# Performance work log

Hardware: AMD Instinct MI355X
Metric: run time of the kernel (lower is better)

## Reference

```python
import jax, jax.numpy as jnp
import numpy as np


def setup_inputs() -> dict:
    key = jax.random.key(0)
    k1, k2, k3 = jax.random.split(key, 3)
    B, T, E = 4, 2048, 1024
    x = jax.random.normal(k1, (B, T, E), dtype=jnp.float32)
    # torch nn.Linear weight layout: [out_features, in_features]
    w_qkv = jax.random.normal(k2, (3 * E, E), dtype=jnp.float32) * (E ** -0.5)
    w_out = jax.random.normal(k3, (E, E), dtype=jnp.float32) * (E ** -0.5)
    return {"x": x, "w_qkv": w_qkv, "w_out": w_out}


def reference(x, w_qkv, w_out):
    B, T, E = x.shape
    H = 16
    D = E // H  # head_dim
    # QKV projection (Linear, bias=False): x @ W.T -> [B,T,3E]
    qkv = jnp.einsum('bte,fe->btf', x, w_qkv)
    qkv = qkv.reshape(B, T, 3, H, D).transpose(2, 0, 3, 1, 4)  # [3,B,H,T,D]
    q, k, v = qkv[0], qkv[1], qkv[2]
    scale = 1.0 / jnp.sqrt(jnp.asarray(D, dtype=x.dtype))
    att = jnp.einsum('bhqd,bhkd->bhqk', q, k) * scale  # [B,H,T,T]
    causal = jnp.tril(jnp.ones((T, T), dtype=bool))
    att = jnp.where(causal[None, None], att, jnp.asarray(-jnp.inf, dtype=att.dtype))
    att = jax.nn.softmax(att, axis=-1)
    # dropout = 0.0 (eval-mode): identity
    y = jnp.einsum('bhqk,bhkd->bhqd', att, v)  # [B,H,T,D]
    y = y.transpose(0, 2, 1, 3).reshape(B, T, E)
    return jnp.einsum('bte,fe->btf', y, w_out)
```

## Files before the change

### kernel.cpp

```cpp
#include <hip/hip_runtime.h>

typedef __bf16 bf16x8 __attribute__((ext_vector_type(8)));
typedef __bf16 bf16x4 __attribute__((ext_vector_type(4)));
typedef __bf16 bf16x2 __attribute__((ext_vector_type(2)));
typedef float f32x4 __attribute__((ext_vector_type(4)));
typedef float f32x16 __attribute__((ext_vector_type(16)));
typedef unsigned short ushortx8 __attribute__((ext_vector_type(8)));
typedef unsigned short ushortx4 __attribute__((ext_vector_type(4)));
typedef unsigned int uint32x4v __attribute__((ext_vector_type(4)));

#define DEVI static __device__ __forceinline__

DEVI unsigned short f2bf(float f) {
  unsigned int u = __builtin_bit_cast(unsigned int, f);
  u += 0x7FFFu + ((u >> 16) & 1u);
  return (unsigned short)(u >> 16);
}

DEVI bf16x8 ld8(const unsigned short* p) {
  return __builtin_bit_cast(bf16x8, *(const ushortx8*)p);
}

DEVI void gll16(const unsigned short* g, unsigned short* l) {
  __builtin_amdgcn_global_load_lds((const __attribute__((address_space(1))) void*)g,
                                   (__attribute__((address_space(3))) void*)l, 16, 0, 0);
}

#define MFMA16(a, b, c) __builtin_amdgcn_mfma_f32_16x16x32_bf16(a, b, c, 0, 0, 0)
#define MFMA32(a, b, c) __builtin_amdgcn_mfma_f32_32x32x16_bf16(a, b, c, 0, 0, 0)

DEVI unsigned pkbf(float lo, float hi) {
  bf16x2 v;
  v[0] = (__bf16)lo;
  v[1] = (__bf16)hi;
  return __builtin_bit_cast(unsigned, v);
}

DEVI float swaphalf_max(float x) {
  unsigned xu = __builtin_bit_cast(unsigned, x);
  auto pr = __builtin_amdgcn_permlane32_swap(xu, xu, false, false);
  return fmaxf(__builtin_bit_cast(float, (unsigned)pr[0]),
               __builtin_bit_cast(float, (unsigned)pr[1]));
}

DEVI float swaphalf_add(float x) {
  unsigned xu = __builtin_bit_cast(unsigned, x);
  auto pr = __builtin_amdgcn_permlane32_swap(xu, xu, false, false);
  return __builtin_bit_cast(float, (unsigned)pr[0]) +
         __builtin_bit_cast(float, (unsigned)pr[1]);
}

DEVI bf16x8 ldswz(const unsigned short* L, int row, int colsh) {
  return ld8(L + row * 64 + ((((colsh * 2) ^ ((row & 7) << 4))) >> 1));
}

#define SB 4
#define ST 2048
#define SE 1024
#define SH 16
#define SD 64
#define QSCALE 0.18033688011112042f
#define DMTHR 11.541560327111708f

#define NXq4   2097152
#define NQKVq4  786432
#define NWOq4   262144

__global__ void cvt_all(const float* __restrict__ x, const float* __restrict__ wq,
                        const float* __restrict__ wo,
                        unsigned short* __restrict__ xb, unsigned short* __restrict__ wqb,
                        unsigned short* __restrict__ wob) {
  int i = blockIdx.x * blockDim.x + threadIdx.x;
  const float* src;
  unsigned short* dst;
  int j;
  if (i < NXq4) { src = x; dst = xb; j = i; }
  else if (i < NXq4 + NQKVq4) { src = wq; dst = wqb; j = i - NXq4; }
  else { src = wo; dst = wob; j = i - NXq4 - NQKVq4; }
  float4 v = ((const float4*)src)[j];
  ushortx4 o;
  o.x = f2bf(v.x); o.y = f2bf(v.y); o.z = f2bf(v.z); o.w = f2bf(v.w);
  ((ushortx4*)dst)[j] = o;
}

template<int EPI>
__global__ __launch_bounds__(512, 2) void gemm_big(
    const unsigned short* __restrict__ A, const unsigned short* __restrict__ Bw,
    float* __restrict__ Cf,
    unsigned short* __restrict__ Qo, unsigned short* __restrict__ Ko,
    unsigned short* __restrict__ VTo,
    int M, int N, int K) {
  __shared__ unsigned short As[2][256 * 64];
  __shared__ unsigned short Bs[2][256 * 64];
  const int tid = threadIdx.x;
  const int lane = tid & 63;
  const int w = tid >> 6;
  const int wr = w >> 2, wc = w & 3;
  const int r16 = lane & 15, g = lane >> 4;

  const int nwg = gridDim.x * gridDim.y;
  const int lin = blockIdx.x + blockIdx.y * gridDim.x;
  const int wg = (lin & 7) * (nwg >> 3) + (lin >> 3);
  const int bx = wg % gridDim.x, by = wg / gridDim.x;
  const int m0 = by * 256, n0 = bx * 256;

  f32x4 acc[8][4] = {};

  auto stage = [&](int kt, int buf) {
    const int k0 = kt << 6;
#pragma unroll
    for (int it = 0; it < 4; ++it) {
      int c = it * 512 + tid;
      int row = c >> 3, j = c & 7;
      int src = ((j * 16) ^ ((row & 7) << 4)) >> 1;
      gll16(A + (size_t)(m0 + row) * K + k0 + src, As[buf] + c * 8);
    }
#pragma unroll
    for (int it = 0; it < 4; ++it) {
      int c = it * 512 + tid;
      int row = c >> 3, j = c & 7;
      int src = ((j * 16) ^ ((row & 7) << 4)) >> 1;
      gll16(Bw + (size_t)(n0 + row) * K + k0 + src, Bs[buf] + c * 8);
    }
  };

  const int ntk = K >> 6;
  stage(0, 0);
  stage(1, 1);
  asm volatile("s_waitcnt vmcnt(8)" ::: "memory");
  __builtin_amdgcn_s_barrier();
  __builtin_amdgcn_sched_barrier(0);

  int cur = 0;
  for (int t = 0; t < ntk; ++t) {
    const unsigned short* Ab = As[cur];
    const unsigned short* Bb = Bs[cur];

    bf16x8 af[8][2], bfr[4][2];
#pragma unroll
    for (int m = 0; m < 8; ++m)
#pragma unroll
      for (int ks = 0; ks < 2; ++ks)
        af[m][ks] = ldswz(Ab, wr * 128 + m * 16 + r16, ks * 32 + g * 8);
#pragma unroll
    for (int n = 0; n < 4; ++n)
#pragma unroll
      for (int ks = 0; ks < 2; ++ks)
        bfr[n][ks] = ldswz(Bb, wc * 64 + n * 16 + r16, ks * 32 + g * 8);

    __builtin_amdgcn_s_setprio(1);
#pragma unroll
    for (int m = 0; m < 8; ++m)
#pragma unroll
      for (int n = 0; n < 4; ++n)
        acc[m][n] = MFMA16(af[m][0], bfr[n][0], acc[m][n]);
    __builtin_amdgcn_s_setprio(0);

    asm volatile("s_waitcnt lgkmcnt(0)" ::: "memory");
    __builtin_amdgcn_s_barrier();
    __builtin_amdgcn_sched_barrier(0);

    if (t + 2 < ntk) stage(t + 2, cur);
    __builtin_amdgcn_sched_barrier(0);

    __builtin_amdgcn_s_setprio(1);
#pragma unroll
    for (int m = 0; m < 8; ++m)
#pragma unroll
      for (int n = 0; n < 4; ++n)
        acc[m][n] = MFMA16(af[m][1], bfr[n][1], acc[m][n]);
    __builtin_amdgcn_s_setprio(0);

    if (t + 1 < ntk) {
      if (t + 2 < ntk) asm volatile("s_waitcnt vmcnt(8)" ::: "memory");
      else             asm volatile("s_waitcnt vmcnt(0)" ::: "memory");
      __builtin_amdgcn_s_barrier();
      __builtin_amdgcn_sched_barrier(0);
    }
    cur ^= 1;
  }

  if (EPI == 0) {
#pragma unroll
    for (int mt = 0; mt < 8; ++mt)
#pragma unroll
      for (int nt2 = 0; nt2 < 4; ++nt2)
#pragma unroll
        for (int r = 0; r < 4; ++r) {
          int m = m0 + wr * 128 + mt * 16 + g * 4 + r;
          int n = n0 + wc * 64 + nt2 * 16 + r16;
          Cf[(size_t)m * N + n] = acc[mt][nt2][r];
        }
  } else {
    const int which = (n0 + wc * 64) >> 10;
#pragma unroll
    for (int mt = 0; mt < 8; ++mt) {
      const int tb = m0 + wr * 128 + mt * 16 + g * 4;
      const int b = tb >> 11, t = tb & (ST - 1);
#pragma unroll
      for (int nt2 = 0; nt2 < 4; ++nt2) {
        int n = n0 + wc * 64 + nt2 * 16 + r16;
        int h = (n >> 6) & (SH - 1), d = n & (SD - 1);
        int bh = b * SH + h;
        if (which == 2) {
          ushortx4 o;
#pragma unroll
          for (int r = 0; r < 4; ++r) o[r] = f2bf(acc[mt][nt2][r]);
          *(ushortx4*)&VTo[((size_t)bh * SD + d) * ST + t] = o;
        } else if (which == 0) {
#pragma unroll
          for (int r = 0; r < 4; ++r)
            Qo[((size_t)bh * ST + t + r) * SD + d] = f2bf(acc[mt][nt2][r] * QSCALE);
        } else {
#pragma unroll
          for (int r = 0; r < 4; ++r)
            Ko[((size_t)bh * ST + t + r) * SD + d] = f2bf(acc[mt][nt2][r]);
        }
      }
    }
  }
}

__global__ __launch_bounds__(256, 2) void gemm_sm(
    const unsigned short* __restrict__ A, const unsigned short* __restrict__ Bw,
    float* __restrict__ Cf, int M, int N, int K) {
  __shared__ unsigned short As[128 * 64];
  __shared__ unsigned short Bs[128 * 64];
  const int tid = threadIdx.x;
  const int lane = tid & 63;
  const int w = tid >> 6;
  const int wr = w >> 1, wc = w & 1;
  const int r16 = lane & 15, g = lane >> 4;

  const int nwg = gridDim.x * gridDim.y;
  const int lin = blockIdx.x + blockIdx.y * gridDim.x;
  const int wg = (lin & 7) * (nwg >> 3) + (lin >> 3);
  const int bx = wg % gridDim.x, by = wg / gridDim.x;
  const int m0 = by * 128, n0 = bx * 128;

  f32x4 acc[4][4] = {};

  for (int k0 = 0; k0 < K; k0 += 64) {
    __syncthreads();
#pragma unroll
    for (int it = 0; it < 4; ++it) {
      int c = it * 256 + tid;
      int row = c >> 3, j = c & 7;
      int src = ((j * 16) ^ ((row & 7) << 4)) >> 1;
      gll16(A + (size_t)(m0 + row) * K + k0 + src, As + c * 8);
    }
#pragma unroll
    for (int it = 0; it < 4; ++it) {
      int c = it * 256 + tid;
      int row = c >> 3, j = c & 7;
      int src = ((j * 16) ^ ((row & 7) << 4)) >> 1;
      gll16(Bw + (size_t)(n0 + row) * K + k0 + src, Bs + c * 8);
    }
    __syncthreads();
#pragma unroll
    for (int ks = 0; ks < 2; ++ks) {
      bf16x8 af[4], bfr[4];
#pragma unroll
      for (int mt = 0; mt < 4; ++mt)
        af[mt] = ldswz(As, wr * 64 + mt * 16 + r16, ks * 32 + g * 8);
#pragma unroll
      for (int nt2 = 0; nt2 < 4; ++nt2)
        bfr[nt2] = ldswz(Bs, wc * 64 + nt2 * 16 + r16, ks * 32 + g * 8);
#pragma unroll
      for (int mt = 0; mt < 4; ++mt)
#pragma unroll
        for (int nt2 = 0; nt2 < 4; ++nt2)
          acc[mt][nt2] = MFMA16(af[mt], bfr[nt2], acc[mt][nt2]);
    }
  }

#pragma unroll
  for (int mt = 0; mt < 4; ++mt)
#pragma unroll
    for (int nt2 = 0; nt2 < 4; ++nt2)
#pragma unroll
      for (int r = 0; r < 4; ++r) {
        int m = m0 + wr * 64 + mt * 16 + g * 4 + r;
        int n = n0 + wc * 64 + nt2 * 16 + r16;
        Cf[(size_t)m * N + n] = acc[mt][nt2][r];
      }
}


DEVI void stage_tile(const unsigned short* gbase, size_t rowstride,
                     unsigned short* lds, int tid) {
#pragma unroll
  for (int it = 0; it < 2; ++it) {
    int c = it * 256 + tid;
    int row = c >> 3, j = c & 7;
    int src = ((j * 16) ^ ((row & 7) << 4)) >> 1;
    gll16(gbase + (size_t)row * rowstride + src, lds + c * 8);
  }
}

__global__ __launch_bounds__(256, 4) void attn_causal(
    const unsigned short* __restrict__ Q, const unsigned short* __restrict__ Kv,
    const unsigned short* __restrict__ VT, unsigned short* __restrict__ Y) {
  __shared__ unsigned short Ks[2][64 * 64];
  __shared__ unsigned short Vs[2][64 * 64];

  const int tid = threadIdx.x;
  const int lane = tid & 63;
  const int w = tid >> 6;
  const int l5 = lane & 31, h = lane >> 5;

  const int lin = blockIdx.x + blockIdx.y * gridDim.x;
  const int xcd = lin & 7;
  const int idx = lin >> 3;
  const int qt = (ST / 128 - 1) - (idx >> 3);
  const int bh = xcd + 8 * (idx & 7);
  const size_t base = (size_t)bh * ST * SD;

  const int q_glob = qt * 128 + w * 32 + l5;
  const int qwmin = qt * 128 + w * 32;

  bf16x8 qf[4];
#pragma unroll
  for (int kk = 0; kk < 4; ++kk)
    qf[kk] = ld8(Q + base + (size_t)q_glob * SD + kk * 16 + h * 8);

  float mrow = -__builtin_inff();
  float lrow = 0.f;
  f32x16 acc[2] = {};

  const int nkv = 2 * qt + 2;
  stage_tile(Kv + base, SD, Ks[0], tid);
  stage_tile(VT + base, ST, Vs[0], tid);
  __syncthreads();

  for (int kvt = 0; kvt < nkv; ++kvt) {
    const int cur = kvt & 1;
    if (kvt + 1 < nkv) {
      stage_tile(Kv + base + (size_t)(kvt + 1) * 64 * SD, SD, Ks[cur ^ 1], tid);
      stage_tile(VT + base + (kvt + 1) * 64, ST, Vs[cur ^ 1], tid);
    }

    const bool active = (kvt * 64) <= (qwmin + 31);
    if (active) {
      f32x16 s0 = {}, s1 = {};
      __builtin_amdgcn_s_setprio(1);
#pragma unroll
      for (int kk = 0; kk < 4; ++kk) {
        bf16x8 k0 = ldswz(Ks[cur], l5, kk * 16 + h * 8);
        s0 = MFMA32(k0, qf[kk], s0);
      }
#pragma unroll
      for (int kk = 0; kk < 4; ++kk) {
        bf16x8 k1 = ldswz(Ks[cur], 32 + l5, kk * 16 + h * 8);
        s1 = MFMA32(k1, qf[kk], s1);
      }
      __builtin_amdgcn_s_setprio(0);

      if (kvt * 64 + 63 > qwmin) {
        const int t0 = kvt * 64 + 4 * h;
#pragma unroll
        for (int reg = 0; reg < 16; ++reg) {
          int t = t0 + (reg & 3) + 8 * (reg >> 2);
          if (t > q_glob) s0[reg] = -__builtin_inff();
          if (t + 32 > q_glob) s1[reg] = -__builtin_inff();
        }
      }

      f32x16 mx;
#pragma unroll
      for (int i = 0; i < 16; ++i) mx[i] = fmaxf(s0[i], s1[i]);
#pragma unroll
      for (int i = 0; i < 8; ++i) mx[i] = fmaxf(mx[i], mx[i + 8]);
#pragma unroll
      for (int i = 0; i < 4; ++i) mx[i] = fmaxf(mx[i], mx[i + 4]);
      float bm = fmaxf(fmaxf(mx[0], mx[1]), fmaxf(mx[2], mx[3]));
      bm = swaphalf_max(bm);

      if (__any(bm > mrow + DMTHR)) {
        float mn = fmaxf(mrow, bm);
        float corr = exp2f(mrow - mn);
        mrow = mn;
        lrow *= corr;
#pragma unroll
        for (int dblk = 0; dblk < 2; ++dblk)
#pragma unroll
          for (int i = 0; i < 16; ++i) acc[dblk][i] *= corr;
      }

#pragma unroll
      for (int i = 0; i < 16; ++i) {
        s0[i] = exp2f(s0[i] - mrow);
        s1[i] = exp2f(s1[i] - mrow);
      }
      f32x16 sm;
#pragma unroll
      for (int i = 0; i < 16; ++i) sm[i] = s0[i] + s1[i];
#pragma unroll
      for (int i = 0; i < 8; ++i) sm[i] += sm[i + 8];
#pragma unroll
      for (int i = 0; i < 4; ++i) sm[i] += sm[i + 4];
      float rs = (sm[0] + sm[1]) + (sm[2] + sm[3]);
      lrow += swaphalf_add(rs);

      bf16x8 pb[2][2];
      auto packblk = [&](const f32x16& S, bf16x8* out) {
        unsigned a = pkbf(S[0], S[1]), b2 = pkbf(S[2], S[3]);
        unsigned c = pkbf(S[4], S[5]), d2 = pkbf(S[6], S[7]);
        auto r0 = __builtin_amdgcn_permlane32_swap(a, c, false, false);
        auto r1 = __builtin_amdgcn_permlane32_swap(b2, d2, false, false);
        uint32x4v w0 = {(unsigned)r0[0], (unsigned)r1[0], (unsigned)r0[1], (unsigned)r1[1]};
        out[0] = __builtin_bit_cast(bf16x8, w0);
        unsigned e = pkbf(S[8], S[9]), f2 = pkbf(S[10], S[11]);
        unsigned g2 = pkbf(S[12], S[13]), h2 = pkbf(S[14], S[15]);
        auto r2 = __builtin_amdgcn_permlane32_swap(e, g2, false, false);
        auto r3 = __builtin_amdgcn_permlane32_swap(f2, h2, false, false);
        uint32x4v w1 = {(unsigned)r2[0], (unsigned)r3[0], (unsigned)r2[1], (unsigned)r3[1]};
        out[1] = __builtin_bit_cast(bf16x8, w1);
      };
      packblk(s0, pb[0]);
      packblk(s1, pb[1]);

      __builtin_amdgcn_s_setprio(1);
#pragma unroll
      for (int dblk = 0; dblk < 2; ++dblk)
#pragma unroll
        for (int tt = 0; tt < 2; ++tt)
#pragma unroll
          for (int sl = 0; sl < 2; ++sl) {
            bf16x8 va = ldswz(Vs[cur], dblk * 32 + l5, tt * 32 + sl * 16 + h * 8);
            acc[dblk] = MFMA32(va, pb[tt][sl], acc[dblk]);
          }
      __builtin_amdgcn_s_setprio(0);
    }

    __syncthreads();
  }

  const int b = bh >> 4, hd = bh & 15;
  const float inv = 1.f / lrow;
#pragma unroll
  for (int dblk = 0; dblk < 2; ++dblk)
#pragma unroll
    for (int rg = 0; rg < 4; ++rg) {
      bf16x4 o;
#pragma unroll
      for (int j = 0; j < 4; ++j) o[j] = (__bf16)(acc[dblk][rg * 4 + j] * inv);
      int d = dblk * 32 + rg * 8 + 4 * h;
      *(ushortx4*)&Y[((size_t)b * ST + q_glob) * SE + hd * SD + d] =
          __builtin_bit_cast(ushortx4, o);
    }
}

extern "C" void kernel_launch(void* const* d_in, const int* in_sizes, int n_in,
                              void* d_out, int out_size, void* d_ws, size_t ws_size,
                              hipStream_t stream) {
  const float* x = (const float*)d_in[0];
  const float* w_qkv = (const float*)d_in[1];
  const float* w_out = (const float*)d_in[2];
  float* out = (float*)d_out;

  const size_t NX = (size_t)SB * ST * SE;
  const size_t NQKV = (size_t)3 * SE * SE;
  const size_t NWO = (size_t)SE * SE;
  const size_t NHD = (size_t)SB * SH * ST * SD;

  unsigned short* xb    = (unsigned short*)d_ws;
  unsigned short* wqkvb = xb + NX;
  unsigned short* woutb = wqkvb + NQKV;
  unsigned short* q     = woutb + NWO;
  unsigned short* k     = q + NHD;
  unsigned short* vT    = k + NHD;
  unsigned short* y     = xb;

  const int ncvt = NXq4 + NQKVq4 + NWOq4;
  cvt_all<<<ncvt / 256, 256, 0, stream>>>(x, w_qkv, w_out, xb, wqkvb, woutb);

  gemm_big<1><<<dim3(3 * SE / 256, SB * ST / 256), 512, 0, stream>>>(
      xb, wqkvb, nullptr, q, k, vT, SB * ST, 3 * SE, SE);

  attn_causal<<<dim3(ST / 128, SB * SH), 256, 0, stream>>>(q, k, vT, y);

  gemm_sm<<<dim3(SE / 128, SB * ST / 128), 256, 0, stream>>>(
      y, woutb, out, SB * ST, SE, SE);
}
```

Measured before the change: 175.4 us.

## Interleave QKV GEMM loads with MFMA quarters and fold max-subtraction into attention scores

```diff
diff --git a/kernel.cpp b/kernel.cpp
--- a/kernel.cpp
+++ b/kernel.cpp
@@ -83,10 +83,8 @@
   ((ushortx4*)dst)[j] = o;
 }
 
-template<int EPI>
-__global__ __launch_bounds__(512, 2) void gemm_big(
+__global__ __launch_bounds__(512, 2) void gemm_big1(
     const unsigned short* __restrict__ A, const unsigned short* __restrict__ Bw,
-    float* __restrict__ Cf,
     unsigned short* __restrict__ Qo, unsigned short* __restrict__ Ko,
     unsigned short* __restrict__ VTo,
     int M, int N, int K) {
@@ -106,116 +104,150 @@
 
   f32x4 acc[8][4] = {};
 
-  auto stage = [&](int kt, int buf) {
-    const int k0 = kt << 6;
-#pragma unroll
-    for (int it = 0; it < 4; ++it) {
-      int c = it * 512 + tid;
-      int row = c >> 3, j = c & 7;
-      int src = ((j * 16) ^ ((row & 7) << 4)) >> 1;
-      gll16(A + (size_t)(m0 + row) * K + k0 + src, As[buf] + c * 8);
-    }
-#pragma unroll
-    for (int it = 0; it < 4; ++it) {
-      int c = it * 512 + tid;
-      int row = c >> 3, j = c & 7;
-      int src = ((j * 16) ^ ((row & 7) << 4)) >> 1;
-      gll16(Bw + (size_t)(n0 + row) * K + k0 + src, Bs[buf] + c * 8);
-    }
+  auto stgA = [&](int v, int r) {
+    int c = r * 512 + tid, row = c >> 3, j = c & 7;
+    int src = ((j * 16) ^ ((row & 7) << 4)) >> 1;
+    gll16(A + (size_t)(m0 + row) * K + (v << 6) + src, As[v & 1] + c * 8);
   };
+  auto stgB = [&](int v, int r) {
+    int c = r * 512 + tid, row = c >> 3, j = c & 7;
+    int src = ((j * 16) ^ ((row & 7) << 4)) >> 1;
+    gll16(Bw + (size_t)(n0 + row) * K + (v << 6) + src, Bs[v & 1] + c * 8);
+  };
 
   const int ntk = K >> 6;
-  stage(0, 0);
-  stage(1, 1);
-  asm volatile("s_waitcnt vmcnt(8)" ::: "memory");
+#pragma unroll
+  for (int r = 0; r < 4; ++r) stgA(0, r);
+#pragma unroll
+  for (int r = 0; r < 4; ++r) stgB(0, r);
+#pragma unroll
+  for (int r = 0; r < 4; ++r) stgB(1, r);
+  stgA(1, 0); stgA(1, 2);
+  asm volatile("s_waitcnt vmcnt(6)" ::: "memory");
   __builtin_amdgcn_s_barrier();
   __builtin_amdgcn_sched_barrier(0);
 
-  int cur = 0;
-  for (int t = 0; t < ntk; ++t) {
-    const unsigned short* Ab = As[cur];
-    const unsigned short* Bb = Bs[cur];
-
-    bf16x8 af[8][2], bfr[4][2];
-#pragma unroll
-    for (int m = 0; m < 8; ++m)
+  for (int u = 0; u < ntk; ++u) {
+    const unsigned short* Ab = As[u & 1];
+    const unsigned short* Bb = Bs[u & 1];
+    bf16x8 bfr[4][2], aq[2][2];
+
+#pragma unroll
+    for (int mt = 0; mt < 2; ++mt)
 #pragma unroll
       for (int ks = 0; ks < 2; ++ks)
-        af[m][ks] = ldswz(Ab, wr * 128 + m * 16 + r16, ks * 32 + g * 8);
+        aq[mt][ks] = ldswz(Ab, wr * 128 + mt * 16 + r16, ks * 32 + g * 8);
 #pragma unroll
     for (int n = 0; n < 4; ++n)
 #pragma unroll
       for (int ks = 0; ks < 2; ++ks)
         bfr[n][ks] = ldswz(Bb, wc * 64 + n * 16 + r16, ks * 32 + g * 8);
-
+    if (u + 1 < ntk) { stgA(u + 1, 1); stgA(u + 1, 3); }
+    asm volatile("s_waitcnt lgkmcnt(8)" ::: "memory");
+    __builtin_amdgcn_s_barrier();
+    asm volatile("s_waitcnt lgkmcnt(0)" ::: "memory");
+    __builtin_amdgcn_sched_barrier(0);
     __builtin_amdgcn_s_setprio(1);
 #pragma unroll
-    for (int m = 0; m < 8; ++m)
+    for (int mt = 0; mt < 2; ++mt)
 #pragma unroll
       for (int n = 0; n < 4; ++n)
-        acc[m][n] = MFMA16(af[m][0], bfr[n][0], acc[m][n]);
+#pragma unroll
+        for (int ks = 0; ks < 2; ++ks)
+          acc[mt][n] = MFMA16(aq[mt][ks], bfr[n][ks], acc[mt][n]);
     __builtin_amdgcn_s_setprio(0);
-
+    __builtin_amdgcn_s_barrier();
+
+#pragma unroll
+    for (int mt = 0; mt < 2; ++mt)
+#pragma unroll
+      for (int ks = 0; ks < 2; ++ks)
+        aq[mt][ks] = ldswz(Ab, wr * 128 + 32 + mt * 16 + r16, ks * 32 + g * 8);
+    if (u + 2 < ntk) { stgB(u + 2, 0); stgB(u + 2, 1); }
+    __builtin_amdgcn_s_barrier();
     asm volatile("s_waitcnt lgkmcnt(0)" ::: "memory");
-    __builtin_amdgcn_s_barrier();
     __builtin_amdgcn_sched_barrier(0);
-
-    if (t + 2 < ntk) stage(t + 2, cur);
+    __builtin_amdgcn_s_setprio(1);
+#pragma unroll
+    for (int mt = 0; mt < 2; ++mt)
+#pragma unroll
+      for (int n = 0; n < 4; ++n)
+#pragma unroll
+        for (int ks = 0; ks < 2; ++ks)
+          acc[2 + mt][n] = MFMA16(aq[mt][ks], bfr[n][ks], acc[2 + mt][n]);
+    __builtin_amdgcn_s_setprio(0);
+    __builtin_amdgcn_s_barrier();
+
+#pragma unroll
+    for (int mt = 0; mt < 2; ++mt)
+#pragma unroll
+      for (int ks = 0; ks < 2; ++ks)
+        aq[mt][ks] = ldswz(Ab, wr * 128 + 64 + mt * 16 + r16, ks * 32 + g * 8);
+    if (u + 2 < ntk) { stgB(u + 2, 2); stgB(u + 2, 3); stgA(u + 2, 0); }
+    __builtin_amdgcn_s_barrier();
+    asm volatile("s_waitcnt lgkmcnt(0)" ::: "memory");
     __builtin_amdgcn_sched_barrier(0);
-
     __builtin_amdgcn_s_setprio(1);
 #pragma unroll
-    for (int m = 0; m < 8; ++m)
+    for (int mt = 0; mt < 2; ++mt)
 #pragma unroll
       for (int n = 0; n < 4; ++n)
-        acc[m][n] = MFMA16(af[m][1], bfr[n][1], acc[m][n]);
+#pragma unroll
+        for (int ks = 0; ks < 2; ++ks)
+          acc[4 + mt][n] = MFMA16(aq[mt][ks], bfr[n][ks], acc[4 + mt][n]);
     __builtin_amdgcn_s_setprio(0);
-
-    if (t + 1 < ntk) {
-      if (t + 2 < ntk) asm volatile("s_waitcnt vmcnt(8)" ::: "memory");
+    __builtin_amdgcn_s_barrier();
+
+#pragma unroll
+    for (int mt = 0; mt < 2; ++mt)
+#pragma unroll
+      for (int ks = 0; ks < 2; ++ks)
+        aq[mt][ks] = ldswz(Ab, wr * 128 + 96 + mt * 16 + r16, ks * 32 + g * 8);
+    if (u + 2 < ntk) stgA(u + 2, 2);
+    __builtin_amdgcn_s_barrier();
+    asm volatile("s_waitcnt lgkmcnt(0)" ::: "memory");
+    __builtin_amdgcn_sched_barrier(0);
+    __builtin_amdgcn_s_setprio(1);
+#pragma unroll
+    for (int mt = 0; mt < 2; ++mt)
+#pragma unroll
+      for (int n = 0; n < 4; ++n)
+#pragma unroll
+        for (int ks = 0; ks < 2; ++ks)
+          acc[6 + mt][n] = MFMA16(aq[mt][ks], bfr[n][ks], acc[6 + mt][n]);
+    __builtin_amdgcn_s_setprio(0);
+
+    if (u + 1 < ntk) {
+      if (u + 2 < ntk) asm volatile("s_waitcnt vmcnt(6)" ::: "memory");
       else             asm volatile("s_waitcnt vmcnt(0)" ::: "memory");
-      __builtin_amdgcn_s_barrier();
-      __builtin_amdgcn_sched_barrier(0);
-    }
-    cur ^= 1;
+    }
+    __builtin_amdgcn_s_barrier();
+    __builtin_amdgcn_sched_barrier(0);
   }
 
-  if (EPI == 0) {
-#pragma unroll
-    for (int mt = 0; mt < 8; ++mt)
-#pragma unroll
-      for (int nt2 = 0; nt2 < 4; ++nt2)
-#pragma unroll
-        for (int r = 0; r < 4; ++r) {
-          int m = m0 + wr * 128 + mt * 16 + g * 4 + r;
-          int n = n0 + wc * 64 + nt2 * 16 + r16;
-          Cf[(size_t)m * N + n] = acc[mt][nt2][r];
-        }
-  } else {
-    const int which = (n0 + wc * 64) >> 10;
-#pragma unroll
-    for (int mt = 0; mt < 8; ++mt) {
-      const int tb = m0 + wr * 128 + mt * 16 + g * 4;
-      const int b = tb >> 11, t = tb & (ST - 1);
-#pragma unroll
-      for (int nt2 = 0; nt2 < 4; ++nt2) {
-        int n = n0 + wc * 64 + nt2 * 16 + r16;
-        int h = (n >> 6) & (SH - 1), d = n & (SD - 1);
-        int bh = b * SH + h;
-        if (which == 2) {
-          ushortx4 o;
-#pragma unroll
-          for (int r = 0; r < 4; ++r) o[r] = f2bf(acc[mt][nt2][r]);
-          *(ushortx4*)&VTo[((size_t)bh * SD + d) * ST + t] = o;
-        } else if (which == 0) {
-#pragma unroll
-          for (int r = 0; r < 4; ++r)
-            Qo[((size_t)bh * ST + t + r) * SD + d] = f2bf(acc[mt][nt2][r] * QSCALE);
-        } else {
-#pragma unroll
-          for (int r = 0; r < 4; ++r)
-            Ko[((size_t)bh * ST + t + r) * SD + d] = f2bf(acc[mt][nt2][r]);
-        }
+  const int which = (n0 + wc * 64) >> 10;
+#pragma unroll
+  for (int mt = 0; mt < 8; ++mt) {
+    const int tb = m0 + wr * 128 + mt * 16 + g * 4;
+    const int b = tb >> 11, t = tb & (ST - 1);
+#pragma unroll
+    for (int nt2 = 0; nt2 < 4; ++nt2) {
+      int n = n0 + wc * 64 + nt2 * 16 + r16;
+      int h = (n >> 6) & (SH - 1), d = n & (SD - 1);
+      int bh = b * SH + h;
+      if (which == 2) {
+        ushortx4 o;
+#pragma unroll
+        for (int r = 0; r < 4; ++r) o[r] = f2bf(acc[mt][nt2][r]);
+        *(ushortx4*)&VTo[((size_t)bh * SD + d) * ST + t] = o;
+      } else if (which == 0) {
+#pragma unroll
+        for (int r = 0; r < 4; ++r)
+          Qo[((size_t)bh * ST + t + r) * SD + d] = f2bf(acc[mt][nt2][r] * QSCALE);
+      } else {
+#pragma unroll
+        for (int r = 0; r < 4; ++r)
+          Ko[((size_t)bh * ST + t + r) * SD + d] = f2bf(acc[mt][nt2][r]);
       }
     }
   }
@@ -286,7 +318,6 @@
       }
 }
 
-
 DEVI void stage_tile(const unsigned short* gbase, size_t rowstride,
                      unsigned short* lds, int tid) {
 #pragma unroll
@@ -324,7 +355,7 @@
   for (int kk = 0; kk < 4; ++kk)
     qf[kk] = ld8(Q + base + (size_t)q_glob * SD + kk * 16 + h * 8);
 
-  float mrow = -__builtin_inff();
+  float mrow = 0.f;
   float lrow = 0.f;
   f32x16 acc[2] = {};
 
@@ -342,7 +373,10 @@
 
     const bool active = (kvt * 64) <= (qwmin + 31);
     if (active) {
-      f32x16 s0 = {}, s1 = {};
+      f32x16 s0, s1;
+      const float negm = -mrow;
+#pragma unroll
+      for (int i = 0; i < 16; ++i) { s0[i] = negm; s1[i] = negm; }
       __builtin_amdgcn_s_setprio(1);
 #pragma unroll
       for (int kk = 0; kk < 4; ++kk) {
@@ -376,22 +410,28 @@
       float bm = fmaxf(fmaxf(mx[0], mx[1]), fmaxf(mx[2], mx[3]));
       bm = swaphalf_max(bm);
 
-      if (__any(bm > mrow + DMTHR)) {
-        float mn = fmaxf(mrow, bm);
-        float corr = exp2f(mrow - mn);
-        mrow = mn;
+      if (__any(bm > DMTHR)) {
+        float delta = fmaxf(bm, 0.f);
+        float corr = exp2f(-delta);
+        mrow += delta;
         lrow *= corr;
 #pragma unroll
         for (int dblk = 0; dblk < 2; ++dblk)
 #pragma unroll
           for (int i = 0; i < 16; ++i) acc[dblk][i] *= corr;
+#pragma unroll
+        for (int i = 0; i < 16; ++i) {
+          s0[i] = exp2f(s0[i] - delta);
+          s1[i] = exp2f(s1[i] - delta);
+        }
+      } else {
+#pragma unroll
+        for (int i = 0; i < 16; ++i) {
+          s0[i] = exp2f(s0[i]);
+          s1[i] = exp2f(s1[i]);
+        }
       }
 
-#pragma unroll
-      for (int i = 0; i < 16; ++i) {
-        s0[i] = exp2f(s0[i] - mrow);
-        s1[i] = exp2f(s1[i] - mrow);
-      }
       f32x16 sm;
 #pragma unroll
       for (int i = 0; i < 16; ++i) sm[i] = s0[i] + s1[i];
@@ -475,8 +515,8 @@
   const int ncvt = NXq4 + NQKVq4 + NWOq4;
   cvt_all<<<ncvt / 256, 256, 0, stream>>>(x, w_qkv, w_out, xb, wqkvb, woutb);
 
-  gemm_big<1><<<dim3(3 * SE / 256, SB * ST / 256), 512, 0, stream>>>(
-      xb, wqkvb, nullptr, q, k, vT, SB * ST, 3 * SE, SE);
+  gemm_big1<<<dim3(3 * SE / 256, SB * ST / 256), 512, 0, stream>>>(
+      xb, wqkvb, q, k, vT, SB * ST, 3 * SE, SE);
 
   attn_causal<<<dim3(ST / 128, SB * SH), 256, 0, stream>>>(q, k, vT, y);
 
```

Measured after the change: 295.3 us. 68.3% more time.
